# Optimization experiments

Hardware: AMD Instinct MI355X
Metric: run time of the kernel (lower is better)

Reference implementation:

```python
import jax, jax.numpy as jnp
import numpy as np

N_NODES = 20000
N_EDGES = 320000
NODE_IN = 64
EDGE_IN = 16
H = 256
NUM_GRAPHS = 64


def _linear_params(key, fan_in, fan_out):
    # torch nn.Linear default init: U(-1/sqrt(fan_in), 1/sqrt(fan_in))
    s = 1.0 / np.sqrt(fan_in)
    kw, kb = jax.random.split(key)
    w = jax.random.uniform(kw, (fan_in, fan_out), minval=-s, maxval=s, dtype=jnp.float32)
    b = jax.random.uniform(kb, (fan_out,), minval=-s, maxval=s, dtype=jnp.float32)
    return w, b


def setup_inputs() -> dict:
    key = jax.random.key(0)
    ks = jax.random.split(key, 20)
    inp = {}
    inp["x"] = jax.random.normal(ks[0], (N_NODES, NODE_IN), dtype=jnp.float32)
    inp["edge_index"] = jax.random.randint(ks[1], (2, N_EDGES), 0, N_NODES)
    inp["batch"] = jnp.sort(jax.random.randint(ks[2], (N_NODES,), 0, NUM_GRAPHS))
    inp["edge_attr"] = jax.random.normal(ks[3], (N_EDGES, EDGE_IN), dtype=jnp.float32)
    # edge_mlp: Linear(edge_in,256) -> ReLU -> Linear(256,256)
    inp["ew1"], inp["eb1"] = _linear_params(ks[4], EDGE_IN, H)
    inp["ew2"], inp["eb2"] = _linear_params(ks[5], H, H)
    # GINEConv internal edge projections: Linear(edge_dim=256 -> in_channels)
    inp["le1_w"], inp["le1_b"] = _linear_params(ks[6], H, NODE_IN)
    inp["le2_w"], inp["le2_b"] = _linear_params(ks[7], H, H)
    # nn1: Linear(node_in,256) -> ReLU -> Linear(256,256)
    inp["n1w1"], inp["n1b1"] = _linear_params(ks[8], NODE_IN, H)
    inp["n1w2"], inp["n1b2"] = _linear_params(ks[9], H, H)
    # nn2: Linear(256,256) -> ReLU -> Linear(256,256)
    inp["n2w1"], inp["n2b1"] = _linear_params(ks[10], H, H)
    inp["n2w2"], inp["n2b2"] = _linear_params(ks[11], H, H)
    # readout MLP and heads
    inp["l1w"], inp["l1b"] = _linear_params(ks[12], H, 128)
    inp["l2w"], inp["l2b"] = _linear_params(ks[13], 128, 64)
    inp["hs_w"], inp["hs_b"] = _linear_params(ks[14], 64, 1)
    inp["hp_w"], inp["hp_b"] = _linear_params(ks[15], 64, 1)
    inp["hn_w"], inp["hn_b"] = _linear_params(ks[16], 64, 1)
    return inp


def _gine_conv(x, src, dst, e_proj, w1, b1, w2, b2):
    # message: ReLU(x_j + projected edge feature), scatter-sum at target i
    msg = jax.nn.relu(x[src] + e_proj)                      # [E, d]
    aggr = jax.ops.segment_sum(msg, dst, num_segments=N_NODES)  # [N, d]
    h = x + aggr                                            # eps = 0
    h = jax.nn.relu(h @ w1 + b1) @ w2 + b2                  # GIN MLP
    return h


def reference(x, edge_index, batch, edge_attr,
              ew1, eb1, ew2, eb2,
              le1_w, le1_b, le2_w, le2_b,
              n1w1, n1b1, n1w2, n1b2,
              n2w1, n2b1, n2w2, n2b2,
              l1w, l1b, l2w, l2b,
              hs_w, hs_b, hp_w, hp_b, hn_w, hn_b):
    src, dst = edge_index[0], edge_index[1]
    # edge MLP
    ea = jax.nn.relu(edge_attr @ ew1 + eb1) @ ew2 + eb2     # [E, 256]
    # conv1 (+outer ReLU)
    h = jax.nn.relu(_gine_conv(x, src, dst, ea @ le1_w + le1_b, n1w1, n1b1, n1w2, n1b2))
    # conv2 (+outer ReLU)
    h = jax.nn.relu(_gine_conv(h, src, dst, ea @ le2_w + le2_b, n2w1, n2b1, n2w2, n2b2))
    # global mean pool over graphs
    sums = jax.ops.segment_sum(h, batch, num_segments=NUM_GRAPHS)        # [G, 256]
    cnts = jax.ops.segment_sum(jnp.ones((h.shape[0],), h.dtype), batch, num_segments=NUM_GRAPHS)
    g = sums / jnp.maximum(cnts, 1.0)[:, None]
    g = jax.nn.relu(g @ l1w + l1b)
    g = jax.nn.relu(g @ l2w + l2b)
    logS = (g @ hs_w + hs_b)[:, 0]
    logP = (g @ hp_w + hp_b)[:, 0]
    nr = (g @ hn_w + hn_b)[:, 0]
    return logS, logP, nr
```

## Files before the change

kernel.cpp:

```cpp
#include <hip/hip_runtime.h>

constexpr int NN  = 20000;
constexpr int NE  = 320000;
constexpr int NG  = 64;

typedef _Float16 f16x8v __attribute__((ext_vector_type(8)));
typedef float    f32x4v __attribute__((ext_vector_type(4)));

constexpr size_t OFF_B1C    = 16384;
constexpr size_t OFF_B2C    = 81984;
constexpr size_t OFF_AGGR1  = 82240;
constexpr size_t OFF_AGGR2  = 1362240;
constexpr size_t OFF_H1H    = 6482240;
constexpr size_t OFF_BN1A   = 9042240;
constexpr size_t OFF_BN1B   = 9050432;
constexpr size_t OFF_BN2A   = 9083200;
constexpr size_t OFF_BN2B   = 9115968;
constexpr size_t OFF_BPE    = 9148736;
constexpr size_t OFF_XH     = 9152832;
constexpr size_t OFF_POOL   = 11602240;
constexpr size_t OFF_CNT    = 11618624;
constexpr size_t OFF_CURSOR = 11618688;
constexpr size_t OFF_ROWPTR = 11638688;
constexpr size_t OFF_PERM   = 11658689;
constexpr size_t OFF_BP1    = 11978752;
constexpr size_t OFF_BP2    = 11986944;

template <int KIN, int NOUT>
__device__ __forceinline__ void mfma_gemm64(const _Float16* t_h,
                                            const _Float16* __restrict__ Bp,
                                            f32x4v (&acc)[4][NOUT / 64],
                                            int w, int lane) {
  const int q = lane >> 4, li = lane & 15;
  constexpr int KSTEPS = KIN / 32;
  constexpr int NTW = NOUT / 64;
  for (int s8 = 0; s8 < KSTEPS; ++s8) {
    f16x8v af[4];
#pragma unroll
    for (int m = 0; m < 4; ++m) {
      int r = 16 * m + li;
      int gl = 4 * s8 + q;
      af[m] = *(const f16x8v*)&t_h[r * KIN + ((gl ^ (r & 7)) << 3)];
    }
#pragma unroll
    for (int nl = 0; nl < NTW; ++nl) {
      int ng = w * NTW + nl;
      f16x8v bf = *(const f16x8v*)&Bp[(size_t)((ng * KSTEPS + s8) * 64 + lane) * 8];
#pragma unroll
      for (int m = 0; m < 4; ++m)
        acc[m][nl] = __builtin_amdgcn_mfma_f32_16x16x32_f16(af[m], bf, acc[m][nl], 0, 0, 0);
    }
  }
}

template <int NTW>
__device__ __forceinline__ void bias_init(f32x4v (&acc)[4][NTW],
                                          const float* __restrict__ b, int w, int li) {
#pragma unroll
  for (int nl = 0; nl < NTW; ++nl) {
    float bv = b[(w * NTW + nl) * 16 + li];
#pragma unroll
    for (int m = 0; m < 4; ++m) { f32x4v t = {bv, bv, bv, bv}; acc[m][nl] = t; }
  }
}

__device__ __forceinline__ void pack_direct(const float* __restrict__ W,
                                            _Float16* __restrict__ Bp,
                                            int t, int ksteps, int nout, int kreal) {
  int lane = t & 63;
  int s = (t >> 6) % ksteps;
  int ng = t / (64 * ksteps);
  int kbase = 32 * s + 8 * (lane >> 4);
  int col = 16 * ng + (lane & 15);
  f16x8v v;
#pragma unroll
  for (int e = 0; e < 8; ++e)
    v[e] = (kbase + e < kreal) ? (_Float16)W[(size_t)(kbase + e) * nout + col]
                               : (_Float16)0.f;
  *(f16x8v*)&Bp[(size_t)t * 8] = v;
}

__device__ __forceinline__ void pack_fold(const float* __restrict__ ew2,
                                          const float* __restrict__ lew,
                                          _Float16* __restrict__ Bp,
                                          int t, int nout) {
  int lane = t & 63;
  int s = (t >> 6) & 7;
  int ng = t >> 9;
  int kbase = 32 * s + 8 * (lane >> 4);
  int col = 16 * ng + (lane & 15);
  f16x8v v;
#pragma unroll
  for (int e = 0; e < 8; ++e) {
    const float* wr = &ew2[(size_t)(kbase + e) * 256];
    float sacc = 0.f;
    for (int k2 = 0; k2 < 256; ++k2) sacc = fmaf(wr[k2], lew[(size_t)k2 * nout + col], sacc);
    v[e] = (_Float16)sacc;
  }
  *(f16x8v*)&Bp[(size_t)t * 8] = v;
}

constexpr int PR_XH   = 0;
constexpr int PR_BP1  = PR_XH + 160000;
constexpr int PR_BP2  = PR_BP1 + 2048;
constexpr int PR_N1A  = PR_BP2 + 8192;
constexpr int PR_N1B  = PR_N1A + 2048;
constexpr int PR_N2A  = PR_N1B + 8192;
constexpr int PR_N2B  = PR_N2A + 8192;
constexpr int PR_BPE  = PR_N2B + 8192;
constexpr int PR_B1C  = PR_BPE + 1024;
constexpr int PR_B2C  = PR_B1C + 64;
constexpr int PR_CNT  = PR_B2C + 256;
constexpr int PR_DEG  = PR_CNT + 64;
constexpr int PR_END  = PR_DEG + NE;

__global__ __launch_bounds__(256) void prep_all(
    const float* __restrict__ ew1, const float* __restrict__ eb1,
    const float* __restrict__ ew2, const float* __restrict__ eb2,
    const float* __restrict__ le1w, const float* __restrict__ le1b,
    const float* __restrict__ le2w, const float* __restrict__ le2b,
    const float* __restrict__ n1w1, const float* __restrict__ n1w2,
    const float* __restrict__ n2w1, const float* __restrict__ n2w2,
    const float* __restrict__ x, const int* __restrict__ batch,
    const int* __restrict__ eidx,
    _Float16* __restrict__ Bp1, _Float16* __restrict__ Bp2,
    _Float16* __restrict__ BpN1a, _Float16* __restrict__ BpN1b,
    _Float16* __restrict__ BpN2a, _Float16* __restrict__ BpN2b,
    _Float16* __restrict__ Bpe,
    float* __restrict__ b1c, float* __restrict__ b2c,
    _Float16* __restrict__ xh, float* __restrict__ cnts,
    int* __restrict__ deg) {
  int idx = blockIdx.x * 256 + threadIdx.x;
  if (idx >= PR_END) return;
  if (idx >= PR_DEG) {
    int e = idx - PR_DEG;
    atomicAdd(&deg[eidx[NE + e]], 1);
  } else if (idx < PR_BP1) {
    int t = idx - PR_XH;
    float4 a = *(const float4*)&x[(size_t)t * 8];
    float4 b = *(const float4*)&x[(size_t)t * 8 + 4];
    f16x8v v;
    v[0] = (_Float16)a.x; v[1] = (_Float16)a.y; v[2] = (_Float16)a.z; v[3] = (_Float16)a.w;
    v[4] = (_Float16)b.x; v[5] = (_Float16)b.y; v[6] = (_Float16)b.z; v[7] = (_Float16)b.w;
    *(f16x8v*)&xh[(size_t)t * 8] = v;
  } else if (idx < PR_BP2) {
    pack_fold(ew2, le1w, Bp1, idx - PR_BP1, 64);
  } else if (idx < PR_N1A) {
    pack_fold(ew2, le2w, Bp2, idx - PR_BP2, 256);
  } else if (idx < PR_N1B) {
    pack_direct(n1w1, BpN1a, idx - PR_N1A, 2, 256, 64);
  } else if (idx < PR_N2A) {
    pack_direct(n1w2, BpN1b, idx - PR_N1B, 8, 256, 256);
  } else if (idx < PR_N2B) {
    pack_direct(n2w1, BpN2a, idx - PR_N2A, 8, 256, 256);
  } else if (idx < PR_BPE) {
    pack_direct(n2w2, BpN2b, idx - PR_N2B, 8, 256, 256);
  } else if (idx < PR_B1C) {
    pack_direct(ew1, Bpe, idx - PR_BPE, 1, 256, 16);
  } else if (idx < PR_B2C) {
    int j = idx - PR_B1C;
    float s = le1b[j];
    for (int k = 0; k < 256; ++k) s = fmaf(eb2[k], le1w[k * 64 + j], s);
    b1c[j] = s;
  } else if (idx < PR_CNT) {
    int j = idx - PR_B2C;
    float s = le2b[j];
    for (int k = 0; k < 256; ++k) s = fmaf(eb2[k], le2w[k * 256 + j], s);
    b2c[j] = s;
  } else {
    int g = idx - PR_CNT;
    int lo = 0, hi = NN;
    while (lo < hi) { int mid = (lo + hi) >> 1; if (batch[mid] < g) lo = mid + 1; else hi = mid; }
    int start = lo;
    lo = 0; hi = NN;
    while (lo < hi) { int mid = (lo + hi) >> 1; if (batch[mid] <= g) lo = mid + 1; else hi = mid; }
    cnts[g] = (float)(lo - start);
  }
}

__global__ __launch_bounds__(1024) void scan_rowptr(int* __restrict__ degcur,
                                                    int* __restrict__ rowptr) {
  __shared__ int wsum[16];
  const int tid = threadIdx.x, lane = tid & 63, w = tid >> 6;
  int base = 0;
  for (int c0 = 0; c0 < NN; c0 += 1024) {
    int i = c0 + tid;
    int v = (i < NN) ? degcur[i] : 0;
    int x = v;
#pragma unroll
    for (int off = 1; off < 64; off <<= 1) {
      int y = __shfl_up(x, off, 64);
      if (lane >= off) x += y;
    }
    if (lane == 63) wsum[w] = x;
    __syncthreads();
    int woff = 0;
    for (int k = 0; k < w; ++k) woff += wsum[k];
    int tot = 0;
    for (int k = 0; k < 16; ++k) tot += wsum[k];
    if (i < NN) {
      int ex = base + woff + x - v;
      rowptr[i] = ex;
      degcur[i] = ex;
    }
    base += tot;
    __syncthreads();
  }
  if (tid == 0) rowptr[NN] = base;
}

__global__ __launch_bounds__(256) void scatter_perm(const int* __restrict__ eidx,
                                                    int* __restrict__ cursor,
                                                    int* __restrict__ perm) {
  int e = blockIdx.x * 256 + threadIdx.x;
  if (e < NE) {
    int d = eidx[NE + e];
    int slot = atomicAdd(&cursor[d], 1);
    perm[slot] = e;
  }
}

template <int NOUT>
__global__ __launch_bounds__(256, 4) void edge_conv_mfma(
    const float* __restrict__ edge_attr, const int* __restrict__ eidx,
    const int* __restrict__ perm,
    const _Float16* __restrict__ Bpe, const float* __restrict__ eb1,
    const _Float16* __restrict__ Bp, const float* __restrict__ bc,
    const _Float16* __restrict__ gat, float* __restrict__ aggr) {
  constexpr int NTW = NOUT / 64;
  constexpr int NG8 = NOUT / 8;
  __shared__ _Float16 ea_h[64 * 40];
  __shared__ _Float16 t_h[64 * 256];
  __shared__ int perm_s[64], src_s[64], dst_s[64];
  const int tid = threadIdx.x;
  const int e0 = blockIdx.x * 64;
  const int lane = tid & 63, w = tid >> 6;
  const int q = lane >> 4, li = lane & 15;

  if (tid < 64) {
    int p = perm[e0 + tid];
    perm_s[tid] = p;
    src_s[tid] = eidx[p];
    dst_s[tid] = eidx[NE + p];
  }
  __syncthreads();
  {
    int e2 = (tid & 127) >> 1, gq = tid & 1;
    if (tid < 128) {
      const float* src = &edge_attr[(size_t)perm_s[e2] * 16 + gq * 8];
      float4 a = *(const float4*)src;
      float4 b = *(const float4*)(src + 4);
      f16x8v v;
      v[0] = (_Float16)a.x; v[1] = (_Float16)a.y; v[2] = (_Float16)a.z; v[3] = (_Float16)a.w;
      v[4] = (_Float16)b.x; v[5] = (_Float16)b.y; v[6] = (_Float16)b.z; v[7] = (_Float16)b.w;
      *(f16x8v*)&ea_h[e2 * 40 + gq * 8] = v;
    } else {
      f16x8v z = {};
      *(f16x8v*)&ea_h[e2 * 40 + 16 + gq * 8] = z;
    }
  }

  f32x4v acct[4][4];
  bias_init<4>(acct, eb1, w, li);
  __syncthreads();
  {
    f16x8v afe[4];
#pragma unroll
    for (int m = 0; m < 4; ++m)
      afe[m] = *(const f16x8v*)&ea_h[(16 * m + li) * 40 + 8 * q];
#pragma unroll
    for (int nl = 0; nl < 4; ++nl) {
      f16x8v bf = *(const f16x8v*)&Bpe[(size_t)((w * 4 + nl) * 64 + lane) * 8];
#pragma unroll
      for (int m = 0; m < 4; ++m)
        acct[m][nl] = __builtin_amdgcn_mfma_f32_16x16x32_f16(afe[m], bf, acct[m][nl], 0, 0, 0);
    }
#pragma unroll
    for (int m = 0; m < 4; ++m)
#pragma unroll
      for (int nl = 0; nl < 4; ++nl)
#pragma unroll
        for (int r = 0; r < 4; ++r) {
          int E = 16 * m + 4 * q + r;
          int p = (((E >> 2) & 3) << 4) | ((E >> 4) << 2) | (E & 3);
          int col = (w * 4 + nl) * 16 + li;
          int g = col >> 3;
          t_h[p * 256 + ((g ^ (p & 7)) << 3) + (col & 7)] =
              (_Float16)fmaxf(acct[m][nl][r], 0.f);
        }
  }

  f32x4v acc[4][NTW];
  bias_init<NTW>(acc, bc, w, li);
  __syncthreads();

  for (int s8 = 0; s8 < 8; ++s8) {
    f16x8v af[4];
#pragma unroll
    for (int m = 0; m < 4; ++m) {
      int r = 16 * m + li;
      int gl = 4 * s8 + q;
      af[m] = *(const f16x8v*)&t_h[r * 256 + ((gl ^ (r & 7)) << 3)];
    }
#pragma unroll
    for (int nl = 0; nl < NTW; ++nl) {
      int ng = w * NTW + nl;
      f16x8v bf = *(const f16x8v*)&Bp[(size_t)((ng * 8 + s8) * 64 + lane) * 8];
#pragma unroll
      for (int m = 0; m < 4; ++m)
        acc[m][nl] = __builtin_amdgcn_mfma_f32_16x16x32_f16(af[m], bf, acc[m][nl], 0, 0, 0);
    }
  }
  __syncthreads();

  for (int c = tid; c < 64 * NG8; c += 256) {
    int e = c / NG8, g = c % NG8;
    f16x8v v = *(const f16x8v*)&gat[(size_t)src_s[e] * NOUT + g * 8];
    int pg = (g & ~7) | ((g + 2 * (e >> 4)) & 7);
    *(f16x8v*)&t_h[e * NOUT + pg * 8] = v;
  }
  __syncthreads();

#pragma unroll
  for (int nl = 0; nl < NTW; ++nl) {
    const int col = (w * NTW + nl) * 16 + li;
    const int gl2 = col >> 3;
    const int pg = (gl2 & ~7) | ((gl2 + 2 * q) & 7);
    const int loff = pg * 8 + (col & 7);
    float run = 0.f;
    int cur = dst_s[16 * q];
#pragma unroll
    for (int m = 0; m < 4; ++m) {
#pragma unroll
      for (int r = 0; r < 4; ++r) {
        int e = 16 * q + 4 * m + r;
        int d = dst_s[e];
        if (d != cur) {
          atomicAdd(&aggr[(size_t)cur * NOUT + col], run);
          run = 0.f; cur = d;
        }
        float xv = (float)t_h[e * NOUT + loff];
        run += fmaxf(xv + acc[m][nl][r], 0.f);
      }
    }
    atomicAdd(&aggr[(size_t)cur * NOUT + col], run);
  }
}

__global__ __launch_bounds__(256, 3) void node_mlp1_mfma(
    const float* __restrict__ x, const float* __restrict__ aggr1,
    const _Float16* __restrict__ BpA, const float* __restrict__ b1,
    const _Float16* __restrict__ BpB, const float* __restrict__ b2,
    _Float16* __restrict__ h1h) {
  __shared__ _Float16 t_h[64 * 256];
  const int tid = threadIdx.x;
  const int i0 = blockIdx.x * 64;
  const int lane = tid & 63, w = tid >> 6;
  const int q = lane >> 4, li = lane & 15;

#pragma unroll
  for (int r2 = 0; r2 < 2; ++r2) {
    int idx = tid + r2 * 256;
    int e = idx >> 3, g = idx & 7;
    int node = i0 + e;
    f16x8v v;
#pragma unroll
    for (int j = 0; j < 8; ++j) v[j] = (_Float16)0.f;
    if (node < NN) {
      float4 a0 = *(const float4*)&x[(size_t)node * 64 + g * 8];
      float4 a1 = *(const float4*)&x[(size_t)node * 64 + g * 8 + 4];
      float4 c0 = *(const float4*)&aggr1[(size_t)node * 64 + g * 8];
      float4 c1 = *(const float4*)&aggr1[(size_t)node * 64 + g * 8 + 4];
      v[0] = (_Float16)(a0.x + c0.x); v[1] = (_Float16)(a0.y + c0.y);
      v[2] = (_Float16)(a0.z + c0.z); v[3] = (_Float16)(a0.w + c0.w);
      v[4] = (_Float16)(a1.x + c1.x); v[5] = (_Float16)(a1.y + c1.y);
      v[6] = (_Float16)(a1.z + c1.z); v[7] = (_Float16)(a1.w + c1.w);
    }
    *(f16x8v*)&t_h[e * 64 + ((g ^ (e & 7)) << 3)] = v;
  }
  __syncthreads();

  f32x4v acc[4][4];
  bias_init<4>(acc, b1, w, li);
  mfma_gemm64<64, 256>(t_h, BpA, acc, w, lane);
  __syncthreads();

#pragma unroll
  for (int m = 0; m < 4; ++m)
#pragma unroll
    for (int nl = 0; nl < 4; ++nl)
#pragma unroll
      for (int r = 0; r < 4; ++r) {
        int row = 16 * m + 4 * q + r;
        int col = (w * 4 + nl) * 16 + li;
        int g = col >> 3;
        t_h[row * 256 + ((g ^ (row & 7)) << 3) + (col & 7)] =
            (_Float16)fmaxf(acc[m][nl][r], 0.f);
      }
  __syncthreads();

  bias_init<4>(acc, b2, w, li);
  mfma_gemm64<256, 256>(t_h, BpB, acc, w, lane);
  __syncthreads();

#pragma unroll
  for (int m = 0; m < 4; ++m)
#pragma unroll
    for (int nl = 0; nl < 4; ++nl)
#pragma unroll
      for (int r = 0; r < 4; ++r) {
        int row = 16 * m + 4 * q + r;
        int col = (w * 4 + nl) * 16 + li;
        t_h[row * 256 + col] = (_Float16)fmaxf(acc[m][nl][r], 0.f);
      }
  __syncthreads();

#pragma unroll
  for (int r8 = 0; r8 < 8; ++r8) {
    int idx = tid + r8 * 256;
    int e = idx >> 5, g = idx & 31;
    int node = i0 + e;
    if (node < NN)
      *(f16x8v*)&h1h[(size_t)node * 256 + g * 8] = *(const f16x8v*)&t_h[e * 256 + g * 8];
  }
}

__global__ __launch_bounds__(256, 3) void node_mlp2_mfma(
    const _Float16* __restrict__ h1h, const float* __restrict__ aggr2,
    const _Float16* __restrict__ BpA, const float* __restrict__ b1,
    const _Float16* __restrict__ BpB, const float* __restrict__ b2,
    const int* __restrict__ batch, float* __restrict__ pool) {
  __shared__ _Float16 t_h[64 * 256];
  __shared__ int batch_s[64];
  const int tid = threadIdx.x;
  const int i0 = blockIdx.x * 64;
  const int lane = tid & 63, w = tid >> 6;
  const int q = lane >> 4, li = lane & 15;

  if (tid < 64) batch_s[tid] = (i0 + tid < NN) ? batch[i0 + tid] : -1;

#pragma unroll
  for (int r8 = 0; r8 < 8; ++r8) {
    int idx = tid + r8 * 256;
    int e = idx >> 5, g = idx & 31;
    int node = i0 + e;
    f16x8v v;
#pragma unroll
    for (int j = 0; j < 8; ++j) v[j] = (_Float16)0.f;
    if (node < NN) {
      f16x8v a = *(const f16x8v*)&h1h[(size_t)node * 256 + g * 8];
      float4 c0 = *(const float4*)&aggr2[(size_t)node * 256 + g * 8];
      float4 c1 = *(const float4*)&aggr2[(size_t)node * 256 + g * 8 + 4];
      v[0] = (_Float16)((float)a[0] + c0.x); v[1] = (_Float16)((float)a[1] + c0.y);
      v[2] = (_Float16)((float)a[2] + c0.z); v[3] = (_Float16)((float)a[3] + c0.w);
      v[4] = (_Float16)((float)a[4] + c1.x); v[5] = (_Float16)((float)a[5] + c1.y);
      v[6] = (_Float16)((float)a[6] + c1.z); v[7] = (_Float16)((float)a[7] + c1.w);
    }
    *(f16x8v*)&t_h[e * 256 + ((g ^ (e & 7)) << 3)] = v;
  }
  __syncthreads();

  f32x4v acc[4][4];
  bias_init<4>(acc, b1, w, li);
  mfma_gemm64<256, 256>(t_h, BpA, acc, w, lane);
  __syncthreads();

#pragma unroll
  for (int m = 0; m < 4; ++m)
#pragma unroll
    for (int nl = 0; nl < 4; ++nl)
#pragma unroll
      for (int r = 0; r < 4; ++r) {
        int row = 16 * m + 4 * q + r;
        int col = (w * 4 + nl) * 16 + li;
        int g = col >> 3;
        t_h[row * 256 + ((g ^ (row & 7)) << 3) + (col & 7)] =
            (_Float16)fmaxf(acc[m][nl][r], 0.f);
      }
  __syncthreads();

  bias_init<4>(acc, b2, w, li);
  mfma_gemm64<256, 256>(t_h, BpB, acc, w, lane);
  __syncthreads();

#pragma unroll
  for (int m = 0; m < 4; ++m)
#pragma unroll
    for (int nl = 0; nl < 4; ++nl)
#pragma unroll
      for (int r = 0; r < 4; ++r) {
        int row = 16 * m + 4 * q + r;
        int col = (w * 4 + nl) * 16 + li;
        t_h[row * 256 + col] = (_Float16)fmaxf(acc[m][nl][r], 0.f);
      }
  __syncthreads();

  float run = 0.f;
  int curg = -2;
  for (int m = 0; m < 64; ++m) {
    int g = batch_s[m];
    if (g != curg) {
      if (curg >= 0) atomicAdd(&pool[curg * 256 + tid], run);
      run = 0.f; curg = g;
    }
    if (g >= 0) run += (float)t_h[m * 256 + tid];
  }
  if (curg >= 0) atomicAdd(&pool[curg * 256 + tid], run);
}

__global__ __launch_bounds__(128) void head_kernel(
    const float* __restrict__ pool, const float* __restrict__ counts,
    const float* __restrict__ l1w, const float* __restrict__ l1b,
    const float* __restrict__ l2w, const float* __restrict__ l2b,
    const float* __restrict__ hs_w, const float* __restrict__ hs_b,
    const float* __restrict__ hp_w, const float* __restrict__ hp_b,
    const float* __restrict__ hn_w, const float* __restrict__ hn_b,
    float* __restrict__ out) {
  const int g = blockIdx.x, tid = threadIdx.x;
  __shared__ float g_s[256], g1_s[128], g2_s[64];
  float cnt = fmaxf(counts[g], 1.0f);
  g_s[tid] = pool[g * 256 + tid] / cnt;
  g_s[tid + 128] = pool[g * 256 + tid + 128] / cnt;
  __syncthreads();
  float s = l1b[tid];
  for (int k = 0; k < 256; ++k) s = fmaf(g_s[k], l1w[k * 128 + tid], s);
  g1_s[tid] = fmaxf(s, 0.f);
  __syncthreads();
  if (tid < 64) {
    float s2 = l2b[tid];
    for (int k = 0; k < 128; ++k) s2 = fmaf(g1_s[k], l2w[k * 64 + tid], s2);
    g2_s[tid] = fmaxf(s2, 0.f);
  }
  __syncthreads();
  if (tid < 64) {
    float v = g2_s[tid];
    float a = v * hs_w[tid], b = v * hp_w[tid], c = v * hn_w[tid];
    for (int off = 32; off > 0; off >>= 1) {
      a += __shfl_down(a, off, 64);
      b += __shfl_down(b, off, 64);
      c += __shfl_down(c, off, 64);
    }
    if (tid == 0) {
      out[g]        = a + hs_b[0];
      out[64 + g]   = b + hp_b[0];
      out[128 + g]  = c + hn_b[0];
    }
  }
}

extern "C" void kernel_launch(void* const* d_in, const int* in_sizes, int n_in,
                              void* d_out, int out_size, void* d_ws, size_t ws_size,
                              hipStream_t stream) {
  (void)in_sizes; (void)n_in; (void)out_size; (void)ws_size;
  const float* x         = (const float*)d_in[0];
  const int*   eidx      = (const int*)d_in[1];
  const int*   batch     = (const int*)d_in[2];
  const float* edge_attr = (const float*)d_in[3];
  const float* ew1  = (const float*)d_in[4];
  const float* eb1  = (const float*)d_in[5];
  const float* ew2  = (const float*)d_in[6];
  const float* eb2  = (const float*)d_in[7];
  const float* le1w = (const float*)d_in[8];
  const float* le1b = (const float*)d_in[9];
  const float* le2w = (const float*)d_in[10];
  const float* le2b = (const float*)d_in[11];
  const float* n1w1 = (const float*)d_in[12];
  const float* n1b1 = (const float*)d_in[13];
  const float* n1w2 = (const float*)d_in[14];
  const float* n1b2 = (const float*)d_in[15];
  const float* n2w1 = (const float*)d_in[16];
  const float* n2b1 = (const float*)d_in[17];
  const float* n2w2 = (const float*)d_in[18];
  const float* n2b2 = (const float*)d_in[19];
  const float* l1w  = (const float*)d_in[20];
  const float* l1b  = (const float*)d_in[21];
  const float* l2w  = (const float*)d_in[22];
  const float* l2b  = (const float*)d_in[23];
  const float* hs_w = (const float*)d_in[24];
  const float* hs_b = (const float*)d_in[25];
  const float* hp_w = (const float*)d_in[26];
  const float* hp_b = (const float*)d_in[27];
  const float* hn_w = (const float*)d_in[28];
  const float* hn_b = (const float*)d_in[29];

  float* ws    = (float*)d_ws;
  float* b1c   = ws + OFF_B1C;
  float* b2c   = ws + OFF_B2C;
  float* aggr1 = ws + OFF_AGGR1;
  float* aggr2 = ws + OFF_AGGR2;
  _Float16* h1h = (_Float16*)(ws + OFF_H1H);
  _Float16* xh  = (_Float16*)(ws + OFF_XH);
  float* pool  = ws + OFF_POOL;
  float* cnts  = ws + OFF_CNT;
  int*   cursor= (int*)ws + OFF_CURSOR;
  int*   rowptr= (int*)ws + OFF_ROWPTR;
  int*   perm  = (int*)ws + OFF_PERM;
  _Float16* Bp1  = (_Float16*)(ws + OFF_BP1);
  _Float16* Bp2  = (_Float16*)(ws + OFF_BP2);
  _Float16* BpN1a = (_Float16*)(ws + OFF_BN1A);
  _Float16* BpN1b = (_Float16*)(ws + OFF_BN1B);
  _Float16* BpN2a = (_Float16*)(ws + OFF_BN2A);
  _Float16* BpN2b = (_Float16*)(ws + OFF_BN2B);
  _Float16* Bpe  = (_Float16*)(ws + OFF_BPE);
  float* out   = (float*)d_out;

  hipMemsetAsync(aggr1, 0, (size_t)NN * 64 * 4, stream);
  hipMemsetAsync(aggr2, 0, (size_t)NN * 256 * 4, stream);
  hipMemsetAsync(pool, 0, (size_t)NG * 256 * 4, stream);
  hipMemsetAsync(cursor, 0, (size_t)NN * 4, stream);

  prep_all<<<(PR_END + 255) / 256, 256, 0, stream>>>(
      ew1, eb1, ew2, eb2, le1w, le1b, le2w, le2b,
      n1w1, n1w2, n2w1, n2w2, x, batch, eidx,
      Bp1, Bp2, BpN1a, BpN1b, BpN2a, BpN2b, Bpe, b1c, b2c, xh, cnts, cursor);

  scan_rowptr<<<1, 1024, 0, stream>>>(cursor, rowptr);
  scatter_perm<<<(NE + 255) / 256, 256, 0, stream>>>(eidx, cursor, perm);

  edge_conv_mfma<64><<<NE / 64, 256, 0, stream>>>(edge_attr, eidx, perm, Bpe, eb1,
                                                  Bp1, b1c, xh, aggr1);
  node_mlp1_mfma<<<(NN + 63) / 64, 256, 0, stream>>>(x, aggr1, BpN1a, n1b1, BpN1b, n1b2, h1h);
  edge_conv_mfma<256><<<NE / 64, 256, 0, stream>>>(edge_attr, eidx, perm, Bpe, eb1,
                                                   Bp2, b2c, h1h, aggr2);
  node_mlp2_mfma<<<(NN + 63) / 64, 256, 0, stream>>>(h1h, aggr2, BpN2a, n2b1, BpN2b, n2b2,
                                                     batch, pool);
  head_kernel<<<NG, 128, 0, stream>>>(pool, cnts, l1w, l1b, l2w, l2b,
                                      hs_w, hs_b, hp_w, hp_b, hn_w, hn_b, out);
}
```

Baseline: 306.9 us.

## Use register shuffles for edge indices and rewrite rowptr scan as blocked serial scan

The edge conv kernel now has every wavefront load the perm, src and dst indices into registers and broadcast them with shuffles, instead of staging them and the edge attributes in shared memory. This removes two block barriers and some LDS, and the occupancy hint is raised from 4 to 5 blocks. The rowptr scan becomes a single pass in which each thread scans a contiguous chunk serially, replacing a loop of barrier-synchronised 1024-wide chunks. In exchange, each wave issues redundant global index loads, and the higher occupancy hint may push the compiler to spill registers.

```diff
diff --git a/kernel.cpp b/kernel.cpp
--- a/kernel.cpp
+++ b/kernel.cpp
@@ -182,31 +182,40 @@
                                                     int* __restrict__ rowptr) {
   __shared__ int wsum[16];
   const int tid = threadIdx.x, lane = tid & 63, w = tid >> 6;
-  int base = 0;
-  for (int c0 = 0; c0 < NN; c0 += 1024) {
-    int i = c0 + tid;
-    int v = (i < NN) ? degcur[i] : 0;
-    int x = v;
-#pragma unroll
-    for (int off = 1; off < 64; off <<= 1) {
-      int y = __shfl_up(x, off, 64);
-      if (lane >= off) x += y;
-    }
-    if (lane == 63) wsum[w] = x;
-    __syncthreads();
-    int woff = 0;
-    for (int k = 0; k < w; ++k) woff += wsum[k];
-    int tot = 0;
-    for (int k = 0; k < 16; ++k) tot += wsum[k];
-    if (i < NN) {
-      int ex = base + woff + x - v;
-      rowptr[i] = ex;
-      degcur[i] = ex;
-    }
-    base += tot;
-    __syncthreads();
-  }
-  if (tid == 0) rowptr[NN] = base;
+  constexpr int PT = (NN + 1023) / 1024;
+  const int base = tid * PT;
+  int loc[PT];
+  int s = 0;
+#pragma unroll
+  for (int i = 0; i < PT; ++i) {
+    int idx = base + i;
+    int v = (idx < NN) ? degcur[idx] : 0;
+    loc[i] = s;
+    s += v;
+  }
+  int x = s;
+#pragma unroll
+  for (int off = 1; off < 64; off <<= 1) {
+    int y = __shfl_up(x, off, 64);
+    if (lane >= off) x += y;
+  }
+  if (lane == 63) wsum[w] = x;
+  __syncthreads();
+  int woff = 0;
+  for (int k = 0; k < w; ++k) woff += wsum[k];
+  int total = 0;
+  for (int k = 0; k < 16; ++k) total += wsum[k];
+  const int ex = woff + x - s;
+#pragma unroll
+  for (int i = 0; i < PT; ++i) {
+    int idx = base + i;
+    if (idx < NN) {
+      int val = ex + loc[i];
+      rowptr[idx] = val;
+      degcur[idx] = val;
+    }
+  }
+  if (tid == 0) rowptr[NN] = total;
 }
 
 __global__ __launch_bounds__(256) void scatter_perm(const int* __restrict__ eidx,
@@ -221,7 +230,7 @@
 }
 
 template <int NOUT>
-__global__ __launch_bounds__(256, 4) void edge_conv_mfma(
+__global__ __launch_bounds__(256, 5) void edge_conv_mfma(
     const float* __restrict__ edge_attr, const int* __restrict__ eidx,
     const int* __restrict__ perm,
     const _Float16* __restrict__ Bpe, const float* __restrict__ eb1,
@@ -229,45 +238,33 @@
     const _Float16* __restrict__ gat, float* __restrict__ aggr) {
   constexpr int NTW = NOUT / 64;
   constexpr int NG8 = NOUT / 8;
-  __shared__ _Float16 ea_h[64 * 40];
   __shared__ _Float16 t_h[64 * 256];
-  __shared__ int perm_s[64], src_s[64], dst_s[64];
   const int tid = threadIdx.x;
   const int e0 = blockIdx.x * 64;
   const int lane = tid & 63, w = tid >> 6;
   const int q = lane >> 4, li = lane & 15;
 
-  if (tid < 64) {
-    int p = perm[e0 + tid];
-    perm_s[tid] = p;
-    src_s[tid] = eidx[p];
-    dst_s[tid] = eidx[NE + p];
-  }
-  __syncthreads();
-  {
-    int e2 = (tid & 127) >> 1, gq = tid & 1;
-    if (tid < 128) {
-      const float* src = &edge_attr[(size_t)perm_s[e2] * 16 + gq * 8];
-      float4 a = *(const float4*)src;
-      float4 b = *(const float4*)(src + 4);
-      f16x8v v;
-      v[0] = (_Float16)a.x; v[1] = (_Float16)a.y; v[2] = (_Float16)a.z; v[3] = (_Float16)a.w;
-      v[4] = (_Float16)b.x; v[5] = (_Float16)b.y; v[6] = (_Float16)b.z; v[7] = (_Float16)b.w;
-      *(f16x8v*)&ea_h[e2 * 40 + gq * 8] = v;
-    } else {
-      f16x8v z = {};
-      *(f16x8v*)&ea_h[e2 * 40 + 16 + gq * 8] = z;
-    }
-  }
+  const int p_r   = perm[e0 + lane];
+  const int src_r = eidx[p_r];
+  const int dst_r = eidx[NE + p_r];
 
   f32x4v acct[4][4];
   bias_init<4>(acct, eb1, w, li);
-  __syncthreads();
   {
     f16x8v afe[4];
 #pragma unroll
-    for (int m = 0; m < 4; ++m)
-      afe[m] = *(const f16x8v*)&ea_h[(16 * m + li) * 40 + 8 * q];
+    for (int m = 0; m < 4; ++m) {
+      int row = __shfl(p_r, 16 * m + li);
+      f16x8v v = {};
+      if (q < 2) {
+        const float* sp = &edge_attr[(size_t)row * 16 + 8 * q];
+        float4 a = *(const float4*)sp;
+        float4 b = *(const float4*)(sp + 4);
+        v[0] = (_Float16)a.x; v[1] = (_Float16)a.y; v[2] = (_Float16)a.z; v[3] = (_Float16)a.w;
+        v[4] = (_Float16)b.x; v[5] = (_Float16)b.y; v[6] = (_Float16)b.z; v[7] = (_Float16)b.w;
+      }
+      afe[m] = v;
+    }
 #pragma unroll
     for (int nl = 0; nl < 4; ++nl) {
       f16x8v bf = *(const f16x8v*)&Bpe[(size_t)((w * 4 + nl) * 64 + lane) * 8];
@@ -315,7 +312,8 @@
 
   for (int c = tid; c < 64 * NG8; c += 256) {
     int e = c / NG8, g = c % NG8;
-    f16x8v v = *(const f16x8v*)&gat[(size_t)src_s[e] * NOUT + g * 8];
+    int srcn = __shfl(src_r, e);
+    f16x8v v = *(const f16x8v*)&gat[(size_t)srcn * NOUT + g * 8];
     int pg = (g & ~7) | ((g + 2 * (e >> 4)) & 7);
     *(f16x8v*)&t_h[e * NOUT + pg * 8] = v;
   }
@@ -328,13 +326,13 @@
     const int pg = (gl2 & ~7) | ((gl2 + 2 * q) & 7);
     const int loff = pg * 8 + (col & 7);
     float run = 0.f;
-    int cur = dst_s[16 * q];
+    int cur = __shfl(dst_r, 16 * q);
 #pragma unroll
     for (int m = 0; m < 4; ++m) {
 #pragma unroll
       for (int r = 0; r < 4; ++r) {
         int e = 16 * q + 4 * m + r;
-        int d = dst_s[e];
+        int d = __shfl(dst_r, e);
         if (d != cur) {
           atomicAdd(&aggr[(size_t)cur * NOUT + col], run);
           run = 0.f; cur = d;
```

Measured after the change: 475.6 us. 55.0% more time.
